# Kernel optimization log

Hardware: AMD Instinct MI355X
Metric: run time of the kernel (lower is better)

## Reference

```python
import math
import jax, jax.numpy as jnp
import numpy as np

TWO_PI = 2.0 * math.pi

def ring_pe(s, K):
    # s: [N] in [0,1). Returns [N, 2K]: interleaved cos/sin harmonics k=1..K.
    k = jnp.arange(1, K + 1, dtype=s.dtype)            # [K]
    ang = TWO_PI * s[:, None] * k[None, :]             # [N, K]
    pe = jnp.stack([jnp.cos(ang), jnp.sin(ang)], axis=-1)  # [N, K, 2]
    return pe.reshape(s.shape[0], 2 * K)

def setup_inputs() -> dict:
    key = jax.random.key(0)
    k1, k2, k3, k4 = jax.random.split(key, 4)
    N, Z, H, K = 2048, 32, 64, 2
    in_dim = 2 * (2 * K) + 2 + Z  # 42
    return {
        "z_g": jax.random.normal(k1, (1, Z), dtype=jnp.float32),
        "s": jax.random.uniform(k2, (N,), dtype=jnp.float32),
        "W1": jax.random.normal(k3, (in_dim, H), dtype=jnp.float32) * (1.0 / math.sqrt(in_dim)),
        "b1": jnp.zeros((H,), dtype=jnp.float32),
        "W2": jax.random.normal(k4, (H, 1), dtype=jnp.float32) * (1.0 / math.sqrt(H)),
        "b2": jnp.zeros((1,), dtype=jnp.float32),
        "K": K,
    }

def reference(z_g, s, W1, b1, W2, b2, K):
    N = s.shape[0]
    pe = ring_pe(s, K)                                  # [N, 2K]
    pe_i = jnp.broadcast_to(pe[:, None, :], (N, N, pe.shape[-1]))
    pe_j = jnp.broadcast_to(pe[None, :, :], (N, N, pe.shape[-1]))
    diff = s[:, None] - s[None, :]
    diff = diff - jnp.floor(diff)
    diff = jnp.minimum(diff, 1.0 - diff)                # circular distance in [0, 0.5]
    diff_pe = jnp.stack([jnp.cos(TWO_PI * diff), jnp.sin(TWO_PI * diff)], axis=-1)  # [N, N, 2]
    zrep = jnp.broadcast_to(z_g.reshape(1, 1, -1), (N, N, z_g.shape[-1]))
    x = jnp.concatenate([pe_i, pe_j, diff_pe, zrep], axis=-1)  # [N, N, 42]
    h = jax.nn.relu(jnp.einsum('ijd,dh->ijh', x, W1) + b1)
    logits = (jnp.einsum('ijh,ho->ijo', h, W2) + b2)[..., 0]   # [N, N]
    logits = 0.5 * (logits + logits.T)
    eye = jnp.eye(N, dtype=bool)
    return jnp.where(eye, jnp.float32(-1e9), logits)
```

## Files before the change

### kernel.cpp

```cpp
#include <hip/hip_runtime.h>
#include <math.h>

#define TWO_PI_F 6.28318530717958647692f

typedef unsigned int u32;
typedef __attribute__((ext_vector_type(4))) float    f4;
typedef __attribute__((ext_vector_type(16))) float   f16v;
typedef __attribute__((ext_vector_type(2))) float    f2;
typedef __attribute__((ext_vector_type(2))) _Float16 h2;
typedef __attribute__((ext_vector_type(4))) _Float16 h4;
typedef __attribute__((ext_vector_type(8))) _Float16 h8;

union B8 { h8 v; h4 q[2]; };
union C2 { u32 w[2]; h4 v; };
union P4 { h2 a[4]; h8 v; };

#if __has_builtin(__builtin_amdgcn_cvt_pkrtz)
__device__ __forceinline__ h2 CVTPK(float a, float b) {
    return __builtin_bit_cast(h2, __builtin_amdgcn_cvt_pkrtz(a, b));
}
#else
__device__ __forceinline__ h2 CVTPK(float a, float b) {
    return (h2){(_Float16)a, (_Float16)b};
}
#endif

__global__ __launch_bounds__(256, 3) void gd_mfma(
    const float* __restrict__ z,  const float* __restrict__ s,
    const float* __restrict__ W1, const float* __restrict__ b1,
    const float* __restrict__ W2, const float* __restrict__ b2v,
    float* __restrict__ out, int N, int NB)
{
    __shared__ __attribute__((aligned(16))) _Float16 Ald[64][24];
    __shared__ __attribute__((aligned(16))) h4 peb[64];
    __shared__ __attribute__((aligned(16))) h2 P2[1024];
    __shared__ __attribute__((aligned(16))) float S[2][32][36];
    __shared__ __attribute__((aligned(16))) f4 strig2[64];
    __shared__ __attribute__((aligned(16))) float w2f[64];
    __shared__ float Lp[12];
    __shared__ float LA[64], LB[64];

    int u = blockIdx.x;
    int M = 2 * NB + 1;
    float disc = (float)(M * M - 8 * u);
    int bi = (int)(((float)M - sqrtf(disc)) * 0.5f);
    if (bi < 0) bi = 0;
    if (bi > NB - 1) bi = NB - 1;
    while (bi > 0 && bi * (M - bi) / 2 > u) --bi;
    while ((bi + 1) * (M - (bi + 1)) / 2 <= u) ++bi;
    int bj = bi + (u - bi * (M - bi) / 2);

    int t    = threadIdx.x;
    int lane = t & 63;

    if (t < 64) {
        int grow = (t < 32) ? (bi * 32 + t) : (bj * 32 + (t - 32));
        float ang = TWO_PI_F * s[grow];
        float c1 = __cosf(ang), s1 = __sinf(ang);
        float c2 = c1 * c1 - s1 * s1, s2 = 2.0f * c1 * s1;
        strig2[t] = (f4){c1, s1, c2, s2};
        peb[t]    = (h4){(_Float16)c1, (_Float16)s1, (_Float16)c2, (_Float16)s2};
        float w2t = W2[t];
        w2f[t] = w2t;

        float zc = b1[t];
#pragma unroll
        for (int zz = 0; zz < 32; ++zz)
            zc = fmaf(z[zz], W1[(10 + zz) * 64 + t], zc);

        h8 row0, row1;
#pragma unroll
        for (int k = 0; k < 8; ++k) row0[k] = (_Float16)W1[k * 64 + t];
        row1 = (h8)0;
        row1[0] = (_Float16)W1[8 * 64 + t];
        row1[1] = (_Float16)W1[9 * 64 + t];
        row1[2] = (_Float16)zc;
        *(h8*)&Ald[t][0] = row0;
        *(h8*)&Ald[t][8] = row1;

        float q25 = 0.25f * w2t;
        float lv[11];
#pragma unroll
        for (int k = 0; k < 8; ++k) lv[k] = (float)row0[k] * q25;
        lv[8]  = (float)row1[0] * q25;
        lv[9]  = (float)row1[1] * q25;
        lv[10] = zc * q25;
#pragma unroll
        for (int off = 32; off; off >>= 1)
#pragma unroll
            for (int k = 0; k < 11; ++k)
                lv[k] += __shfl_xor(lv[k], off);
        if (t == 0) {
#pragma unroll
            for (int k = 0; k < 11; ++k) Lp[k] = lv[k];
        }
    }
    __syncthreads();

    {
        int base = t * 4;
        int il = base >> 5, j0 = base & 31;
        f4 ci = strig2[il];
        P4 pk;
#pragma unroll
        for (int c = 0; c < 4; ++c) {
            f4 cj = strig2[32 + j0 + c];
            float ctv = fmaf(ci.x, cj.x, ci.y * cj.y);
            float stv = fabsf(fmaf(ci.y, cj.x, -(ci.x * cj.y)));
            pk.a[c] = CVTPK(ctv, stv);
        }
        *(h8*)&P2[base] = pk.v;
    }
    if (t < 64) {
        f4 tg = strig2[t];
        LA[t] = fmaf(Lp[0], tg.x, fmaf(Lp[1], tg.y,
                 fmaf(Lp[2], tg.z, fmaf(Lp[3], tg.w, Lp[10]))));
        LB[t] = fmaf(Lp[4], tg.x, fmaf(Lp[5], tg.y,
                 fmaf(Lp[6], tg.z, Lp[7] * tg.w)));
    }

    int n = lane & 31;
    int q = lane >> 5;

    h8 afr[2];
    float w2v[2][16];
#pragma unroll
    for (int H = 0; H < 2; ++H) {
        afr[H] = *(const h8*)&Ald[H * 32 + n][q * 8];
#pragma unroll
        for (int e = 0; e < 16; ++e)
            w2v[H][e] = 0.25f * w2f[(e & 3) + 8 * (e >> 2) + 4 * q + 32 * H];
    }
    __syncthreads();

    int wv   = t >> 6;
    int o    = wv >> 1;
    int base = (wv & 1) * 16;

    h4 pe_inv = peb[32 + n];
    float laneInv = o ? LA[32 + n] : LB[32 + n];
    float Lp8r = Lp[8], Lp9r = Lp[9];

#pragma unroll
    for (int i = 0; i < 8; ++i) {
        int ilA = base + i;
        int ilB = base + i + 8;

        h4 varA = peb[ilA];
        h4 varB = peb[ilB];
        u32 pwA = *(const u32*)&P2[ilA * 32 + n];
        u32 pwB = *(const u32*)&P2[ilB * 32 + n];
        float rowA = o ? LB[ilA] : LA[ilA];
        float rowB = o ? LB[ilB] : LA[ilB];

        B8 bA, bB;
        {
            h4 pa = o ? pe_inv : varA;
            h4 pb = o ? varA : pe_inv;
            C2 cc; cc.w[0] = pwA; cc.w[1] = 0x00003C00u;
            bA.q[0] = q ? cc.v : pa;
            bA.q[1] = q ? (h4)0 : pb;
        }
        {
            h4 pa = o ? pe_inv : varB;
            h4 pb = o ? varB : pe_inv;
            C2 cc; cc.w[0] = pwB; cc.w[1] = 0x00003C00u;
            bB.q[0] = q ? cc.v : pa;
            bB.q[1] = q ? (h4)0 : pb;
        }

        f16v a0A = __builtin_amdgcn_mfma_f32_32x32x16_f16(afr[0], bA.v, (f16v)(0.0f), 0, 0, 0);
        f16v a1A = __builtin_amdgcn_mfma_f32_32x32x16_f16(afr[1], bA.v, (f16v)(0.0f), 0, 0, 0);
        f16v a0B = __builtin_amdgcn_mfma_f32_32x32x16_f16(afr[0], bB.v, (f16v)(0.0f), 0, 0, 0);
        f16v a1B = __builtin_amdgcn_mfma_f32_32x32x16_f16(afr[1], bB.v, (f16v)(0.0f), 0, 0, 0);

        float cA0 = 0.f, cA1 = 0.f, cA2 = 0.f, cA3 = 0.f;
        float cB0 = 0.f, cB1 = 0.f, cB2 = 0.f, cB3 = 0.f;
#pragma unroll
        for (int e = 0; e < 8; ++e) {
            cA0 = fmaf(fabsf(a0A[e]),     w2v[0][e],     cA0);
            cA1 = fmaf(fabsf(a0A[e + 8]), w2v[0][e + 8], cA1);
            cA2 = fmaf(fabsf(a1A[e]),     w2v[1][e],     cA2);
            cA3 = fmaf(fabsf(a1A[e + 8]), w2v[1][e + 8], cA3);
            cB0 = fmaf(fabsf(a0B[e]),     w2v[0][e],     cB0);
            cB1 = fmaf(fabsf(a0B[e + 8]), w2v[0][e + 8], cB1);
            cB2 = fmaf(fabsf(a1B[e]),     w2v[1][e],     cB2);
            cB3 = fmaf(fabsf(a1B[e + 8]), w2v[1][e + 8], cB3);
        }
        float psA = (cA0 + cA1) + (cA2 + cA3);
        float psB = (cB0 + cB1) + (cB2 + cB3);
        psA += __shfl_xor(psA, 32);
        psB += __shfl_xor(psB, 32);

        h2 ppA = __builtin_bit_cast(h2, pwA);
        h2 ppB = __builtin_bit_cast(h2, pwB);
        float linA = rowA + laneInv;
        linA = fmaf((float)ppA[0], Lp8r, linA);
        linA = fmaf((float)ppA[1], Lp9r, linA);
        float linB = rowB + laneInv;
        linB = fmaf((float)ppB[0], Lp8r, linB);
        linB = fmaf((float)ppB[1], Lp9r, linB);
        psA += linA;
        psB += linB;

        if (q == 0) {
            S[o][ilA][n] = psA;
            S[o][ilB][n] = psB;
        }
    }
    __syncthreads();

    float b2 = b2v[0];
    {
        int il = t >> 3;
        int j0 = (t & 7) * 4;
        f4 a = *(const f4*)&S[0][il][j0];
        f4 b = *(const f4*)&S[1][il][j0];
        f4 v;
#pragma unroll
        for (int c = 0; c < 4; ++c) {
            float x = a[c] + b[c] + b2;
            if (bi == bj && il == j0 + c) x = -1e9f;
            v[c] = x;
        }
        *(f4*)&out[(size_t)(bi * 32 + il) * N + bj * 32 + j0] = v;

        if (bj > bi) {
            int jl = t >> 3;
            int i0 = (t & 7) * 4;
            f4 m;
#pragma unroll
            for (int c = 0; c < 4; ++c)
                m[c] = S[0][i0 + c][jl] + S[1][i0 + c][jl] + b2;
            *(f4*)&out[(size_t)(bj * 32 + jl) * N + bi * 32 + i0] = m;
        }
    }
}

extern "C" void kernel_launch(void* const* d_in, const int* in_sizes, int n_in,
                              void* d_out, int out_size, void* d_ws, size_t ws_size,
                              hipStream_t stream) {
    const float* z  = (const float*)d_in[0];
    const float* s  = (const float*)d_in[1];
    const float* W1 = (const float*)d_in[2];
    const float* b1 = (const float*)d_in[3];
    const float* W2 = (const float*)d_in[4];
    const float* b2 = (const float*)d_in[5];
    int N = in_sizes[1];

    float* out = (float*)d_out;
    int NB = N / 32;
    int nblk = NB * (NB + 1) / 2;
    gd_mfma<<<nblk, 256, 0, stream>>>(z, s, W1, b1, W2, b2, out, N, NB);
}
```

Measured before the change: 27.06 us.

## Hoist weight preprocessing into a single-block setup kernel shared by all tiles

The folding of z into the bias, the fp16 packing of the W1 rows, the reduction of the linear-term coefficients and the W2 permutation move out of every block into a one-block setup kernel. Its results go to workspace. The main kernel then loads the MFMA A-fragments and W2 weights straight from global memory (L2-resident) and drops a shared-memory staging step. This removes redundant per-block prologue work (a 32-term dot product, shuffles and global loads repeated over 2080 blocks) at the cost of an extra kernel launch and its dependency.

```diff
diff --git a/kernel.cpp b/kernel.cpp
--- a/kernel.cpp
+++ b/kernel.cpp
@@ -25,19 +25,59 @@
 }
 #endif
 
+__global__ __launch_bounds__(64) void gd_setup(
+    const float* __restrict__ z,  const float* __restrict__ W1,
+    const float* __restrict__ b1, const float* __restrict__ W2,
+    _Float16* __restrict__ wpre, float* __restrict__ Lp,
+    float* __restrict__ w2perm)
+{
+    int t = threadIdx.x;
+
+    float zc = b1[t];
+#pragma unroll
+    for (int zz = 0; zz < 32; ++zz)
+        zc = fmaf(z[zz], W1[(10 + zz) * 64 + t], zc);
+
+    h8 row0, row1;
+#pragma unroll
+    for (int k = 0; k < 8; ++k) row0[k] = (_Float16)W1[k * 64 + t];
+    row1 = (h8)0;
+    row1[0] = (_Float16)W1[8 * 64 + t];
+    row1[1] = (_Float16)W1[9 * 64 + t];
+    row1[2] = (_Float16)zc;
+    *(h8*)&wpre[t * 16]     = row0;
+    *(h8*)&wpre[t * 16 + 8] = row1;
+
+    float q25 = 0.25f * W2[t];
+    float lv[11];
+#pragma unroll
+    for (int k = 0; k < 8; ++k) lv[k] = (float)row0[k] * q25;
+    lv[8]  = (float)row1[0] * q25;
+    lv[9]  = (float)row1[1] * q25;
+    lv[10] = zc * q25;
+#pragma unroll
+    for (int off = 32; off; off >>= 1)
+#pragma unroll
+        for (int k = 0; k < 11; ++k)
+            lv[k] += __shfl_xor(lv[k], off);
+    if (t == 0) {
+#pragma unroll
+        for (int k = 0; k < 11; ++k) Lp[k] = lv[k];
+    }
+
+    int e = t & 15, q_ = (t >> 4) & 1, H = t >> 5;
+    w2perm[t] = 0.25f * W2[(e & 3) + 8 * (e >> 2) + 4 * q_ + 32 * H];
+}
+
 __global__ __launch_bounds__(256, 3) void gd_mfma(
-    const float* __restrict__ z,  const float* __restrict__ s,
-    const float* __restrict__ W1, const float* __restrict__ b1,
-    const float* __restrict__ W2, const float* __restrict__ b2v,
-    float* __restrict__ out, int N, int NB)
+    const float* __restrict__ s,   const _Float16* __restrict__ wpre,
+    const float* __restrict__ Lpg, const float* __restrict__ w2perm,
+    const float* __restrict__ b2v, float* __restrict__ out, int N, int NB)
 {
-    __shared__ __attribute__((aligned(16))) _Float16 Ald[64][24];
     __shared__ __attribute__((aligned(16))) h4 peb[64];
     __shared__ __attribute__((aligned(16))) h2 P2[1024];
     __shared__ __attribute__((aligned(16))) float S[2][32][36];
     __shared__ __attribute__((aligned(16))) f4 strig2[64];
-    __shared__ __attribute__((aligned(16))) float w2f[64];
-    __shared__ float Lp[12];
     __shared__ float LA[64], LB[64];
 
     int u = blockIdx.x;
@@ -52,6 +92,19 @@
 
     int t    = threadIdx.x;
     int lane = t & 63;
+    int n    = lane & 31;
+    int q    = lane >> 5;
+
+    h8 afr[2];
+    f4 w2v4[2][4];
+#pragma unroll
+    for (int H = 0; H < 2; ++H) {
+        afr[H] = *(const h8*)&wpre[(H * 32 + n) * 16 + q * 8];
+#pragma unroll
+        for (int g = 0; g < 4; ++g)
+            w2v4[H][g] = *(const f4*)&w2perm[H * 32 + q * 16 + g * 4];
+    }
+    float Lp8r = Lpg[8], Lp9r = Lpg[9];
 
     if (t < 64) {
         int grow = (t < 32) ? (bi * 32 + t) : (bj * 32 + (t - 32));
@@ -60,40 +113,10 @@
         float c2 = c1 * c1 - s1 * s1, s2 = 2.0f * c1 * s1;
         strig2[t] = (f4){c1, s1, c2, s2};
         peb[t]    = (h4){(_Float16)c1, (_Float16)s1, (_Float16)c2, (_Float16)s2};
-        float w2t = W2[t];
-        w2f[t] = w2t;
-
-        float zc = b1[t];
-#pragma unroll
-        for (int zz = 0; zz < 32; ++zz)
-            zc = fmaf(z[zz], W1[(10 + zz) * 64 + t], zc);
-
-        h8 row0, row1;
-#pragma unroll
-        for (int k = 0; k < 8; ++k) row0[k] = (_Float16)W1[k * 64 + t];
-        row1 = (h8)0;
-        row1[0] = (_Float16)W1[8 * 64 + t];
-        row1[1] = (_Float16)W1[9 * 64 + t];
-        row1[2] = (_Float16)zc;
-        *(h8*)&Ald[t][0] = row0;
-        *(h8*)&Ald[t][8] = row1;
-
-        float q25 = 0.25f * w2t;
-        float lv[11];
-#pragma unroll
-        for (int k = 0; k < 8; ++k) lv[k] = (float)row0[k] * q25;
-        lv[8]  = (float)row1[0] * q25;
-        lv[9]  = (float)row1[1] * q25;
-        lv[10] = zc * q25;
-#pragma unroll
-        for (int off = 32; off; off >>= 1)
-#pragma unroll
-            for (int k = 0; k < 11; ++k)
-                lv[k] += __shfl_xor(lv[k], off);
-        if (t == 0) {
-#pragma unroll
-            for (int k = 0; k < 11; ++k) Lp[k] = lv[k];
-        }
+        LA[t] = fmaf(Lpg[0], c1, fmaf(Lpg[1], s1,
+                 fmaf(Lpg[2], c2, fmaf(Lpg[3], s2, Lpg[10]))));
+        LB[t] = fmaf(Lpg[4], c1, fmaf(Lpg[5], s1,
+                 fmaf(Lpg[6], c2, Lpg[7] * s2)));
     }
     __syncthreads();
 
@@ -111,26 +134,6 @@
         }
         *(h8*)&P2[base] = pk.v;
     }
-    if (t < 64) {
-        f4 tg = strig2[t];
-        LA[t] = fmaf(Lp[0], tg.x, fmaf(Lp[1], tg.y,
-                 fmaf(Lp[2], tg.z, fmaf(Lp[3], tg.w, Lp[10]))));
-        LB[t] = fmaf(Lp[4], tg.x, fmaf(Lp[5], tg.y,
-                 fmaf(Lp[6], tg.z, Lp[7] * tg.w)));
-    }
-
-    int n = lane & 31;
-    int q = lane >> 5;
-
-    h8 afr[2];
-    float w2v[2][16];
-#pragma unroll
-    for (int H = 0; H < 2; ++H) {
-        afr[H] = *(const h8*)&Ald[H * 32 + n][q * 8];
-#pragma unroll
-        for (int e = 0; e < 16; ++e)
-            w2v[H][e] = 0.25f * w2f[(e & 3) + 8 * (e >> 2) + 4 * q + 32 * H];
-    }
     __syncthreads();
 
     int wv   = t >> 6;
@@ -139,7 +142,9 @@
 
     h4 pe_inv = peb[32 + n];
     float laneInv = o ? LA[32 + n] : LB[32 + n];
-    float Lp8r = Lp[8], Lp9r = Lp[9];
+
+    const float* w2v0 = (const float*)&w2v4[0][0];
+    const float* w2v1 = (const float*)&w2v4[1][0];
 
 #pragma unroll
     for (int i = 0; i < 8; ++i) {
@@ -178,14 +183,14 @@
         float cB0 = 0.f, cB1 = 0.f, cB2 = 0.f, cB3 = 0.f;
 #pragma unroll
         for (int e = 0; e < 8; ++e) {
-            cA0 = fmaf(fabsf(a0A[e]),     w2v[0][e],     cA0);
-            cA1 = fmaf(fabsf(a0A[e + 8]), w2v[0][e + 8], cA1);
-            cA2 = fmaf(fabsf(a1A[e]),     w2v[1][e],     cA2);
-            cA3 = fmaf(fabsf(a1A[e + 8]), w2v[1][e + 8], cA3);
-            cB0 = fmaf(fabsf(a0B[e]),     w2v[0][e],     cB0);
-            cB1 = fmaf(fabsf(a0B[e + 8]), w2v[0][e + 8], cB1);
-            cB2 = fmaf(fabsf(a1B[e]),     w2v[1][e],     cB2);
-            cB3 = fmaf(fabsf(a1B[e + 8]), w2v[1][e + 8], cB3);
+            cA0 = fmaf(fabsf(a0A[e]),     w2v0[e],     cA0);
+            cA1 = fmaf(fabsf(a0A[e + 8]), w2v0[e + 8], cA1);
+            cA2 = fmaf(fabsf(a1A[e]),     w2v1[e],     cA2);
+            cA3 = fmaf(fabsf(a1A[e + 8]), w2v1[e + 8], cA3);
+            cB0 = fmaf(fabsf(a0B[e]),     w2v0[e],     cB0);
+            cB1 = fmaf(fabsf(a0B[e + 8]), w2v0[e + 8], cB1);
+            cB2 = fmaf(fabsf(a1B[e]),     w2v1[e],     cB2);
+            cB3 = fmaf(fabsf(a1B[e + 8]), w2v1[e + 8], cB3);
         }
         float psA = (cA0 + cA1) + (cA2 + cA3);
         float psB = (cB0 + cB1) + (cB2 + cB3);
@@ -248,8 +253,14 @@
     const float* b2 = (const float*)d_in[5];
     int N = in_sizes[1];
 
+    _Float16* wpre   = (_Float16*)d_ws;
+    float*    Lp     = (float*)(wpre + 64 * 16);
+    float*    w2perm = Lp + 12;
+
     float* out = (float*)d_out;
     int NB = N / 32;
     int nblk = NB * (NB + 1) / 2;
-    gd_mfma<<<nblk, 256, 0, stream>>>(z, s, W1, b1, W2, b2, out, N, NB);
-}
+
+    gd_setup<<<1, 64, 0, stream>>>(z, W1, b1, W2, wpre, Lp, w2perm);
+    gd_mfma<<<nblk, 256, 0, stream>>>(s, wpre, Lp, w2perm, b2, out, N, NB);
+}
```

Result: slower. 28.85 us (+6.6%).
